# Kernel tuning notes

Hardware: AMD Instinct MI355X
Metric: run time of the kernel (lower is better)

## Reference

```python
import jax, jax.numpy as jnp
import numpy as np
import math

S = 128
EPS = 1e-05

def _rope_seq(x):
    # x: [B, L, 2, s]; rope over dim=1 (sequence), matching torch rope(x, dim=1)
    B, L, two, s = x.shape
    half = s // 2
    pos = jnp.arange(L, dtype=jnp.float32)[:, None]              # [L,1] (one unsqueeze)
    inv_freq = 10000.0 ** (jnp.arange(half, dtype=jnp.float32) / half)
    sinusoid = pos[..., None] * inv_freq[None, None, :]          # [L,1,half]
    sin = jnp.sin(sinusoid)
    cos = jnp.cos(sinusoid)
    x1, x2 = jnp.split(x, 2, axis=-1)
    return jnp.concatenate([x1 * cos - x2 * sin, x2 * cos + x1 * sin], axis=-1)

def setup_inputs() -> dict:
    key = jax.random.key(0)
    ks = jax.random.split(key, 8)
    B, L, D = 8, 1024, 1024
    E = 2 * D
    x = jax.random.normal(ks[0], (B, L, D), dtype=jnp.float32)
    g = jnp.ones((1,), dtype=jnp.float32)
    uv_w = jax.random.normal(ks[1], (2 * E + S, D), dtype=jnp.float32) * 0.02
    gamma = jax.random.uniform(ks[2], (2, S), dtype=jnp.float32)
    beta = jax.random.uniform(ks[3], (2, S), dtype=jnp.float32)
    w_rel = jax.random.uniform(ks[4], (2 * L - 1,), dtype=jnp.float32)
    o_w = jax.random.normal(ks[5], (D, E), dtype=jnp.float32) * 0.02
    res_scale = jnp.ones((D,), dtype=jnp.float32)
    return {"x": x, "g": g, "uv_w": uv_w, "gamma": gamma, "beta": beta,
            "w_rel": w_rel, "o_w": o_w, "res_scale": res_scale}

def reference(x, g, uv_w, gamma, beta, w_rel, o_w, res_scale):
    B, L, D = x.shape
    E = (uv_w.shape[0] - S) // 2
    sqrt_s = math.sqrt(S)
    # ScaleNorm
    norm = jnp.linalg.norm(x, axis=-1, keepdims=True) * (D ** -0.5)
    xn = x / jnp.maximum(norm, EPS) * g
    # gated projection + activation
    uv = jax.nn.silu(xn @ uv_w.T)                               # [B,L,2E+S]
    u = uv[..., :E]
    v = uv[..., E:2 * E]
    base = uv[..., 2 * E:]                                       # [B,L,S]
    base = base[:, :, None, :] * gamma[None, None] + beta        # [B,L,2,S]
    base = _rope_seq(base)
    q = base[:, :, 0]                                            # [B,L,S]
    k = base[:, :, 1]
    qk = jnp.einsum('bis,bjs->bij', q, k)                        # [B,L,L]
    # Toeplitz relative bias: bias[i,j] = w_rel[j - i + L - 1]
    idx = jnp.arange(L)[None, :] - jnp.arange(L)[:, None] + (L - 1)
    qk = qk + w_rel[idx][None]
    kernel = jnp.square(jax.nn.relu(qk / sqrt_s))
    out = u * jnp.einsum('bij,bje->bie', kernel, v)              # [B,L,E]
    out = out @ o_w.T                                            # [B,L,D]
    return x * res_scale + out
```

## Files before the change

### kernel.cpp

```cpp
#include <hip/hip_runtime.h>
#include <hip/hip_bf16.h>
#include <math.h>


typedef __hip_bfloat16 bf16;
using v8s = __attribute__((ext_vector_type(8))) short;
using v4f = __attribute__((ext_vector_type(4))) float;
typedef unsigned short u16;

#define BTCH 8
#define LSEQ 1024
#define DDIM 1024
#define EDIM 2048
#define SDIM 128
#define UVN  4224
#define SLABW 4096
#define BUFW  (4 * SLABW)

__device__ __forceinline__ float ldany(const void* p, size_t i, int bf) {
  return bf ? __bfloat162float(((const bf16*)p)[i]) : ((const float*)p)[i];
}
__device__ __forceinline__ void stany(void* p, size_t i, float v, int bf) {
  if (bf) ((bf16*)p)[i] = __float2bfloat16(v);
  else    ((float*)p)[i] = v;
}
__device__ __forceinline__ u16 f2bf(float x) {
  bf16 b = __float2bfloat16(x);
  return *reinterpret_cast<u16*>(&b);
}
__device__ __forceinline__ float bf2f(u16 u) {
  return __uint_as_float((unsigned)u << 16);
}
__device__ __forceinline__ float silu(float v) {
  return v / (1.0f + __expf(-v));
}

__device__ __forceinline__ void xcd_swz(int& bx, int& by) {
  const int W = gridDim.x;
  const int G = W * gridDim.y;
  const int orig = blockIdx.y * W + blockIdx.x;
  const int xcd = orig & 7;
  const int local = orig >> 3;
  const int chunk = G >> 3;
  if ((G & 7) == 0 && chunk % W == 0) {
    const int R = chunk / W;
    bx = local / R;
    by = xcd * R + local % R;
  } else {
    const int q = G >> 3, r = G & 7;
    const int nid = (xcd < r ? xcd * (q + 1) : r * (q + 1) + (xcd - r) * q)
                    + local;
    bx = nid % W;
    by = nid / W;
  }
}

__device__ __forceinline__ void gld16(const u16* g, u16* l) {
  __builtin_amdgcn_global_load_lds(
      (const __attribute__((address_space(1))) void*)g,
      (__attribute__((address_space(3))) void*)l, 16, 0, 0);
}

__device__ __forceinline__ const v8s* swz_rd(const u16* slab, int row, int q) {
  return (const v8s*)(slab + row * 32 + ((q ^ ((row >> 1) & 3)) << 3));
}

__global__ void detect_kernel(const u16* g16, int* flag) {
  *flag = (g16[0] == 0x3F80) ? 1 : 0;
}

__global__ __launch_bounds__(256) void wsplit_kernel(const void* __restrict__ w,
                                                     u16* __restrict__ whi,
                                                     u16* __restrict__ wlo,
                                                     const int* __restrict__ flagp,
                                                     int n) {
  const int bf = *flagp;
  const size_t i = ((size_t)blockIdx.x * 256 + threadIdx.x) * 8;
  if (i >= (size_t)n) return;
  if (bf) {
    *(uint4*)(whi + i) = *(const uint4*)((const u16*)w + i);
  } else {
    const float* wf = (const float*)w;
    float t[8];
    *(float4*)&t[0] = *(const float4*)(wf + i);
    *(float4*)&t[4] = *(const float4*)(wf + i + 4);
    u16 h[8], l[8];
    #pragma unroll
    for (int j = 0; j < 8; j++) {
      h[j] = f2bf(t[j]);
      l[j] = f2bf(t[j] - bf2f(h[j]));
    }
    *(uint4*)(whi + i) = *(uint4*)&h[0];
    *(uint4*)(wlo + i) = *(uint4*)&l[0];
  }
}

__global__ __launch_bounds__(256) void rmsnorm_kernel(const void* __restrict__ x,
                                                      const void* __restrict__ g,
                                                      u16* __restrict__ xnhi,
                                                      u16* __restrict__ xnlo,
                                                      const int* __restrict__ flagp,
                                                      unsigned long long row0) {
  const int bf = *flagp;
  const int m = blockIdx.x;
  const size_t gbase = (row0 + m) * DDIM;
  float ss = 0.f;
  float vals[4];
  #pragma unroll
  for (int i = 0; i < 4; i++) {
    vals[i] = ldany(x, gbase + threadIdx.x + i * 256, bf);
    ss += vals[i] * vals[i];
  }
  #pragma unroll
  for (int o = 32; o > 0; o >>= 1) ss += __shfl_down(ss, o);
  __shared__ float red[5];
  if ((threadIdx.x & 63) == 0) red[threadIdx.x >> 6] = ss;
  __syncthreads();
  if (threadIdx.x == 0) {
    float tot = red[0] + red[1] + red[2] + red[3];
    float rms = sqrtf(tot * (1.0f / DDIM));
    red[4] = ldany(g, 0, bf) / fmaxf(rms, 1e-5f);
  }
  __syncthreads();
  const float scale = red[4];
  #pragma unroll
  for (int i = 0; i < 4; i++) {
    const size_t idx = (size_t)m * DDIM + threadIdx.x + i * 256;
    float v = vals[i] * scale;
    u16 h = f2bf(v);
    xnhi[idx] = h;
    xnlo[idx] = f2bf(v - bf2f(h));
  }
}

__device__ __forceinline__ void mfma_core(u16* __restrict__ sm,
                                          const u16* __restrict__ AhiG,
                                          const u16* __restrict__ AloG, int lda,
                                          const u16* __restrict__ BhiG,
                                          const u16* __restrict__ BloG, int ldb,
                                          int use_blo, int K, v4f acc[4][4]) {
  const int tid = threadIdx.x;
  const int w = tid >> 6, lane = tid & 63, quad = lane >> 4, lr = lane & 15;
  const int wr = w >> 1, wc = w & 1;
  const int sr0 = w * 16 + (lane >> 2);
  const int sch = lane & 3;

  auto stage = [&](int buf, int kk) {
    u16* lbase = sm + buf * BUFW + w * 512;
    #pragma unroll
    for (int c = 0; c < 2; c++) {
      const int r = sr0 + c * 64;
      const int sc = sch ^ ((r >> 1) & 3);
      u16* ld = lbase + c * 2048;
      const size_t oa = (size_t)r * lda + kk + sc * 8;
      const size_t ob = (size_t)r * ldb + kk + sc * 8;
      gld16(AhiG + oa, ld);
      gld16(AloG + oa, ld + SLABW);
      gld16(BhiG + ob, ld + 2 * SLABW);
      if (use_blo) gld16(BloG + ob, ld + 3 * SLABW);
    }
  };

  stage(0, 0);
  __syncthreads();
  int cur = 0;
  for (int k0 = 0; k0 < K; k0 += 32) {
    if (k0 + 32 < K) stage(cur ^ 1, k0 + 32);
    const u16* sA = sm + cur * BUFW;
    v8s aH[4], aL[4], bh[4], bl[4];
    #pragma unroll
    for (int rt = 0; rt < 4; rt++) {
      const int row = wr * 64 + rt * 16 + lr;
      aH[rt] = *swz_rd(sA, row, quad);
      aL[rt] = *swz_rd(sA + SLABW, row, quad);
    }
    #pragma unroll
    for (int ct = 0; ct < 4; ct++) {
      const int brow = wc * 64 + ct * 16 + lr;
      bh[ct] = *swz_rd(sA + 2 * SLABW, brow, quad);
      if (use_blo) bl[ct] = *swz_rd(sA + 3 * SLABW, brow, quad);
    }
    #pragma unroll
    for (int ct = 0; ct < 4; ct++) {
      #pragma unroll
      for (int rt = 0; rt < 4; rt++)
        acc[rt][ct] = __builtin_amdgcn_mfma_f32_16x16x32_bf16(aH[rt], bh[ct], acc[rt][ct], 0, 0, 0);
      #pragma unroll
      for (int rt = 0; rt < 4; rt++)
        acc[rt][ct] = __builtin_amdgcn_mfma_f32_16x16x32_bf16(aL[rt], bh[ct], acc[rt][ct], 0, 0, 0);
      if (use_blo) {
        #pragma unroll
        for (int rt = 0; rt < 4; rt++)
          acc[rt][ct] = __builtin_amdgcn_mfma_f32_16x16x32_bf16(aH[rt], bl[ct], acc[rt][ct], 0, 0, 0);
      }
    }
    __syncthreads();
    cur ^= 1;
  }
}

template <typename F>
__device__ __forceinline__ void epilogue_rows(const v4f acc[4][4], F body) {
  const int tid = threadIdx.x;
  const int w = tid >> 6, lane = tid & 63;
  const int quad = lane >> 4, lr = lane & 15;
  const int wr = w >> 1, wc = w & 1;
  #pragma unroll
  for (int rt = 0; rt < 4; rt++)
    #pragma unroll
    for (int rg = 0; rg < 4; rg++) {
      const int lrow = wr * 64 + rt * 16 + quad * 4 + rg;
      #pragma unroll
      for (int ct = 0; ct < 4; ct++) {
        const int lcol = wc * 64 + ct * 16 + lr;
        body(lrow, lcol, acc[rt][ct][rg]);
      }
    }
}

__global__ __launch_bounds__(256) void gemm_uv_kernel(const u16* __restrict__ xnhi,
                                                      const u16* __restrict__ xnlo,
                                                      const u16* __restrict__ uvwhi,
                                                      const u16* __restrict__ uvwlo,
                                                      float* __restrict__ u,
                                                      u16* __restrict__ vThi,
                                                      u16* __restrict__ vTlo,
                                                      float* __restrict__ base,
                                                      const int* __restrict__ flagp) {
  __shared__ __align__(16) u16 sm[2 * BUFW];
  const int bf = *flagp;
  int bxi, byi;
  xcd_swz(bxi, byi);
  const int bm = byi * 128, bn = bxi * 128;
  v4f acc[4][4];
  #pragma unroll
  for (int rt = 0; rt < 4; rt++)
    #pragma unroll
    for (int ct = 0; ct < 4; ct++) acc[rt][ct] = (v4f){0.f, 0.f, 0.f, 0.f};
  mfma_core(sm, xnhi + (size_t)bm * DDIM, xnlo + (size_t)bm * DDIM, DDIM,
            uvwhi + (size_t)bn * DDIM, uvwlo + (size_t)bn * DDIM, DDIM,
            bf ? 0 : 1, DDIM, acc);

  if (bn < EDIM) {
    epilogue_rows(acc, [&](int lrow, int lcol, float av) {
      u[(size_t)(bm + lrow) * EDIM + bn + lcol] = silu(av);
    });
  } else if (bn < 2 * EDIM) {
    const int z = bm >> 10, l0 = bm & (LSEQ - 1), e0 = bn - EDIM;
    const int tid = threadIdx.x;
    #pragma unroll
    for (int pass = 0; pass < 2; pass++) {
      __syncthreads();
      epilogue_rows(acc, [&](int lrow, int lcol, float av) {
        const float v = silu(av);
        const u16 hh = f2bf(v);
        sm[lcol * 136 + lrow] = pass ? f2bf(v - bf2f(hh)) : hh;
      });
      __syncthreads();
      u16* dst = pass ? vTlo : vThi;
      const int c = tid >> 1, part = tid & 1;
      const uint4* srcp = (const uint4*)(sm + c * 136 + part * 64);
      uint4* dstp = (uint4*)(dst + ((size_t)z * EDIM + e0 + c) * LSEQ + l0 + part * 64);
      #pragma unroll
      for (int j = 0; j < 8; j++) dstp[j] = srcp[j];
    }
  } else {
    epilogue_rows(acc, [&](int lrow, int lcol, float av) {
      base[(size_t)(bm + lrow) * SDIM + (bn - 2 * EDIM) + lcol] = silu(av);
    });
  }
}

__global__ __launch_bounds__(64) void rope_kernel(const float* __restrict__ base,
                                                  const void* __restrict__ gamma,
                                                  const void* __restrict__ beta,
                                                  u16* __restrict__ qhi,
                                                  u16* __restrict__ qlo,
                                                  u16* __restrict__ khi,
                                                  u16* __restrict__ klo,
                                                  const int* __restrict__ flagp) {
  const int bf = *flagp;
  const int m = blockIdx.x;
  const int pos = m & (LSEQ - 1);
  const int j = threadIdx.x;
  double f = pow(10000.0, (double)j / 64.0);
  double ds, dc;
  sincos((double)pos * f, &ds, &dc);
  const float s = (float)ds, c = (float)dc;
  const float b1 = base[(size_t)m * SDIM + j];
  const float b2 = base[(size_t)m * SDIM + 64 + j];
  {
    float x1 = b1 * ldany(gamma, j, bf) + ldany(beta, j, bf);
    float x2 = b2 * ldany(gamma, 64 + j, bf) + ldany(beta, 64 + j, bf);
    float o1 = x1 * c - x2 * s, o2 = x2 * c + x1 * s;
    u16 h1 = f2bf(o1), h2 = f2bf(o2);
    qhi[(size_t)m * SDIM + j] = h1;      qlo[(size_t)m * SDIM + j] = f2bf(o1 - bf2f(h1));
    qhi[(size_t)m * SDIM + 64 + j] = h2; qlo[(size_t)m * SDIM + 64 + j] = f2bf(o2 - bf2f(h2));
  }
  {
    float x1 = b1 * ldany(gamma, SDIM + j, bf) + ldany(beta, SDIM + j, bf);
    float x2 = b2 * ldany(gamma, SDIM + 64 + j, bf) + ldany(beta, SDIM + 64 + j, bf);
    float o1 = x1 * c - x2 * s, o2 = x2 * c + x1 * s;
    u16 h1 = f2bf(o1), h2 = f2bf(o2);
    khi[(size_t)m * SDIM + j] = h1;      klo[(size_t)m * SDIM + j] = f2bf(o1 - bf2f(h1));
    khi[(size_t)m * SDIM + 64 + j] = h2; klo[(size_t)m * SDIM + 64 + j] = f2bf(o2 - bf2f(h2));
  }
}

__global__ __launch_bounds__(256) void gemm_qk_kernel(const u16* __restrict__ qhi,
                                                      const u16* __restrict__ qlo,
                                                      const u16* __restrict__ khi,
                                                      const u16* __restrict__ klo,
                                                      const void* __restrict__ w_rel,
                                                      u16* __restrict__ kerhi,
                                                      u16* __restrict__ kerlo,
                                                      const int* __restrict__ flagp) {
  __shared__ __align__(16) u16 sm[2 * BUFW];
  const int bf = *flagp;
  const int z = blockIdx.z;
  int bxi, byi;
  xcd_swz(bxi, byi);
  const int bm = byi * 128, bn = bxi * 128;
  v4f acc[4][4];
  #pragma unroll
  for (int rt = 0; rt < 4; rt++)
    #pragma unroll
    for (int ct = 0; ct < 4; ct++) acc[rt][ct] = (v4f){0.f, 0.f, 0.f, 0.f};
  const size_t ao = ((size_t)z * LSEQ + bm) * SDIM;
  const size_t bo = ((size_t)z * LSEQ + bn) * SDIM;
  mfma_core(sm, qhi + ao, qlo + ao, SDIM, khi + bo, klo + bo, SDIM, 1, SDIM, acc);
  const float inv_sqrt_s = 0.08838834764831845f;
  epilogue_rows(acc, [&](int lrow, int lcol, float av) {
    const int gi = bm + lrow, gj = bn + lcol;
    float v = av + ldany(w_rel, gj - gi + (LSEQ - 1), bf);
    v = fmaxf(v, 0.f) * inv_sqrt_s;
    v = v * v;
    const u16 hh = f2bf(v);
    const size_t idx = ((size_t)z * LSEQ + gi) * LSEQ + gj;
    kerhi[idx] = hh;
    kerlo[idx] = f2bf(v - bf2f(hh));
  });
}

__global__ __launch_bounds__(256) void gemm_av_kernel(const u16* __restrict__ kerhi,
                                                      const u16* __restrict__ kerlo,
                                                      const u16* __restrict__ vThi,
                                                      const u16* __restrict__ vTlo,
                                                      const float* __restrict__ u,
                                                      u16* __restrict__ out2hi,
                                                      u16* __restrict__ out2lo) {
  __shared__ __align__(16) u16 sm[2 * BUFW];
  const int z = blockIdx.z;
  int bxi, byi;
  xcd_swz(bxi, byi);
  const int bm = byi * 128, bn = bxi * 128;
  v4f acc[4][4];
  #pragma unroll
  for (int rt = 0; rt < 4; rt++)
    #pragma unroll
    for (int ct = 0; ct < 4; ct++) acc[rt][ct] = (v4f){0.f, 0.f, 0.f, 0.f};
  const size_t ao = ((size_t)z * LSEQ + bm) * LSEQ;
  const size_t bo = ((size_t)z * EDIM + bn) * LSEQ;
  mfma_core(sm, kerhi + ao, kerlo + ao, LSEQ, vThi + bo, vTlo + bo, LSEQ,
            1, LSEQ, acc);
  epilogue_rows(acc, [&](int lrow, int lcol, float av) {
    const size_t grow = (size_t)z * LSEQ + bm + lrow;
    const float v = av * u[grow * EDIM + bn + lcol];
    const u16 hh = f2bf(v);
    out2hi[grow * EDIM + bn + lcol] = hh;
    out2lo[grow * EDIM + bn + lcol] = f2bf(v - bf2f(hh));
  });
}

__global__ __launch_bounds__(256) void gemm_out_kernel(const u16* __restrict__ out2hi,
                                                       const u16* __restrict__ out2lo,
                                                       const u16* __restrict__ owhi,
                                                       const u16* __restrict__ owlo,
                                                       const void* __restrict__ x,
                                                       const void* __restrict__ res_scale,
                                                       void* __restrict__ out,
                                                       const int* __restrict__ flagp,
                                                       unsigned long long row0) {
  __shared__ __align__(16) u16 sm[2 * BUFW];
  const int bf = *flagp;
  int bxi, byi;
  xcd_swz(bxi, byi);
  const int bm = byi * 128, bn = bxi * 128;
  v4f acc[4][4];
  #pragma unroll
  for (int rt = 0; rt < 4; rt++)
    #pragma unroll
    for (int ct = 0; ct < 4; ct++) acc[rt][ct] = (v4f){0.f, 0.f, 0.f, 0.f};
  mfma_core(sm, out2hi + (size_t)bm * EDIM, out2lo + (size_t)bm * EDIM, EDIM,
            owhi + (size_t)bn * EDIM, owlo + (size_t)bn * EDIM, EDIM,
            bf ? 0 : 1, EDIM, acc);
  epilogue_rows(acc, [&](int lrow, int lcol, float av) {
    const size_t gidx = (row0 + bm + lrow) * DDIM + bn + lcol;
    float v = av + ldany(x, gidx, bf) * ldany(res_scale, bn + lcol, bf);
    stany(out, gidx, v, bf);
  });
}

extern "C" void kernel_launch(void* const* d_in, const int* in_sizes, int n_in,
                              void* d_out, int out_size, void* d_ws, size_t ws_size,
                              hipStream_t stream) {
  const void* x         = d_in[0];
  const void* g         = d_in[1];
  const void* uv_w      = d_in[2];
  const void* gamma     = d_in[3];
  const void* beta      = d_in[4];
  const void* w_rel     = d_in[5];
  const void* o_w       = d_in[6];
  const void* res_scale = d_in[7];

  char* ws = (char*)d_ws;
  size_t off = 0;
  int* flag = (int*)(ws + off); off += 256;
  u16* uvwhi = (u16*)(ws + off); off += (size_t)UVN * DDIM * 2;
  u16* uvwlo = (u16*)(ws + off); off += (size_t)UVN * DDIM * 2;
  u16* owhi  = (u16*)(ws + off); off += (size_t)DDIM * EDIM * 2;
  u16* owlo  = (u16*)(ws + off); off += (size_t)DDIM * EDIM * 2;

  int nb = 1;
  for (int cand = 8; cand >= 1; cand >>= 1) {
    size_t need = off + (size_t)cand * 35127296ULL;
    if (ws_size >= need) { nb = cand; break; }
  }
  const int rows = nb * LSEQ;

  u16*   xnhi = (u16*)(ws + off); off += (size_t)rows * DDIM * 2;
  u16*   xnlo = (u16*)(ws + off); off += (size_t)rows * DDIM * 2;
  float* u    = (float*)(ws + off); off += (size_t)rows * EDIM * 4;
  float* base = (float*)(ws + off); off += (size_t)rows * SDIM * 4;
  u16*   qhi  = (u16*)(ws + off); off += (size_t)rows * SDIM * 2;
  u16*   qlo  = (u16*)(ws + off); off += (size_t)rows * SDIM * 2;
  u16*   khi  = (u16*)(ws + off); off += (size_t)rows * SDIM * 2;
  u16*   klo  = (u16*)(ws + off); off += (size_t)rows * SDIM * 2;
  u16*   kerhi= (u16*)(ws + off); off += (size_t)nb * LSEQ * LSEQ * 2;
  u16*   kerlo= (u16*)(ws + off); off += (size_t)nb * LSEQ * LSEQ * 2;
  u16*   vThi = (u16*)(ws + off); off += (size_t)nb * EDIM * LSEQ * 2;
  u16*   vTlo = (u16*)(ws + off); off += (size_t)nb * EDIM * LSEQ * 2;
  u16*   o2hi = (u16*)(ws + off); off += (size_t)rows * EDIM * 2;
  u16*   o2lo = (u16*)(ws + off); off += (size_t)rows * EDIM * 2;

  detect_kernel<<<1, 1, 0, stream>>>((const u16*)g, flag);
  wsplit_kernel<<<(UVN * DDIM) / (8 * 256), 256, 0, stream>>>(uv_w, uvwhi, uvwlo,
                                                              flag, UVN * DDIM);
  wsplit_kernel<<<(DDIM * EDIM) / (8 * 256), 256, 0, stream>>>(o_w, owhi, owlo,
                                                               flag, DDIM * EDIM);

  for (int b = 0; b < BTCH / nb; b++) {
    const unsigned long long row0 = (unsigned long long)b * rows;

    rmsnorm_kernel<<<rows, 256, 0, stream>>>(x, g, xnhi, xnlo, flag, row0);
    {
      dim3 grid(UVN / 128, rows / 128);
      gemm_uv_kernel<<<grid, 256, 0, stream>>>(xnhi, xnlo, uvwhi, uvwlo, u,
                                               vThi, vTlo, base, flag);
    }
    rope_kernel<<<rows, 64, 0, stream>>>(base, gamma, beta, qhi, qlo, khi, klo, flag);
    {
      dim3 grid(LSEQ / 128, LSEQ / 128, nb);
      gemm_qk_kernel<<<grid, 256, 0, stream>>>(qhi, qlo, khi, klo, w_rel,
                                               kerhi, kerlo, flag);
    }
    {
      dim3 grid(EDIM / 128, LSEQ / 128, nb);
      gemm_av_kernel<<<grid, 256, 0, stream>>>(kerhi, kerlo, vThi, vTlo, u,
                                               o2hi, o2lo);
    }
    {
      dim3 grid(DDIM / 128, rows / 128);
      gemm_out_kernel<<<grid, 256, 0, stream>>>(o2hi, o2lo, owhi, owlo, x,
                                                res_scale, d_out, flag, row0);
    }
  }
}
```

Before: 669.0 us.

## Load A operand directly from global into registers, stage only B in LDS

The shared GEMM core now stages only the B operand (hi/lo) through LDS. Each wave reads its A fragments (hi and lo) straight from global memory into registers, double-buffered across two k-steps with a loop unrolled by two. This halves LDS footprint and LDS read traffic and should allow higher occupancy. The cost is more register pressure and uncoalesced-ish 16-byte global loads for A. The A rows are also duplicated across the two column-waves, and the loop assumes K is a multiple of 64.

```diff
diff --git a/kernel.cpp b/kernel.cpp
--- a/kernel.cpp
+++ b/kernel.cpp
@@ -15,7 +15,7 @@
 #define SDIM 128
 #define UVN  4224
 #define SLABW 4096
-#define BUFW  (4 * SLABW)
+#define BUFB  (2 * SLABW)
 
 __device__ __forceinline__ float ldany(const void* p, size_t i, int bf) {
   return bf ? __bfloat162float(((const bf16*)p)[i]) : ((const float*)p)[i];
@@ -145,57 +145,59 @@
   const int sr0 = w * 16 + (lane >> 2);
   const int sch = lane & 3;
 
-  auto stage = [&](int buf, int kk) {
-    u16* lbase = sm + buf * BUFW + w * 512;
+  auto stageB = [&](int buf, int kk) {
+    u16* lbase = sm + buf * BUFB + w * 512;
     #pragma unroll
     for (int c = 0; c < 2; c++) {
       const int r = sr0 + c * 64;
       const int sc = sch ^ ((r >> 1) & 3);
       u16* ld = lbase + c * 2048;
-      const size_t oa = (size_t)r * lda + kk + sc * 8;
       const size_t ob = (size_t)r * ldb + kk + sc * 8;
-      gld16(AhiG + oa, ld);
-      gld16(AloG + oa, ld + SLABW);
-      gld16(BhiG + ob, ld + 2 * SLABW);
-      if (use_blo) gld16(BloG + ob, ld + 3 * SLABW);
+      gld16(BhiG + ob, ld);
+      if (use_blo) gld16(BloG + ob, ld + SLABW);
     }
   };
 
-  stage(0, 0);
-  __syncthreads();
-  int cur = 0;
-  for (int k0 = 0; k0 < K; k0 += 32) {
-    if (k0 + 32 < K) stage(cur ^ 1, k0 + 32);
-    const u16* sA = sm + cur * BUFW;
-    v8s aH[4], aL[4], bh[4], bl[4];
+  auto prefA = [&](v8s aH[4], v8s aL[4], int kk) {
     #pragma unroll
     for (int rt = 0; rt < 4; rt++) {
-      const int row = wr * 64 + rt * 16 + lr;
-      aH[rt] = *swz_rd(sA, row, quad);
-      aL[rt] = *swz_rd(sA + SLABW, row, quad);
-    }
+      const size_t ro = (size_t)(wr * 64 + rt * 16 + lr) * lda + kk + quad * 8;
+      aH[rt] = *(const v8s*)(AhiG + ro);
+      aL[rt] = *(const v8s*)(AloG + ro);
+    }
+  };
+
+  auto compute = [&](const u16* sB, const v8s aH[4], const v8s aL[4]) {
     #pragma unroll
     for (int ct = 0; ct < 4; ct++) {
       const int brow = wc * 64 + ct * 16 + lr;
-      bh[ct] = *swz_rd(sA + 2 * SLABW, brow, quad);
-      if (use_blo) bl[ct] = *swz_rd(sA + 3 * SLABW, brow, quad);
-    }
-    #pragma unroll
-    for (int ct = 0; ct < 4; ct++) {
+      const v8s bh = *swz_rd(sB, brow, quad);
       #pragma unroll
       for (int rt = 0; rt < 4; rt++)
-        acc[rt][ct] = __builtin_amdgcn_mfma_f32_16x16x32_bf16(aH[rt], bh[ct], acc[rt][ct], 0, 0, 0);
+        acc[rt][ct] = __builtin_amdgcn_mfma_f32_16x16x32_bf16(aH[rt], bh, acc[rt][ct], 0, 0, 0);
       #pragma unroll
       for (int rt = 0; rt < 4; rt++)
-        acc[rt][ct] = __builtin_amdgcn_mfma_f32_16x16x32_bf16(aL[rt], bh[ct], acc[rt][ct], 0, 0, 0);
+        acc[rt][ct] = __builtin_amdgcn_mfma_f32_16x16x32_bf16(aL[rt], bh, acc[rt][ct], 0, 0, 0);
       if (use_blo) {
+        const v8s bl = *swz_rd(sB + SLABW, brow, quad);
         #pragma unroll
         for (int rt = 0; rt < 4; rt++)
-          acc[rt][ct] = __builtin_amdgcn_mfma_f32_16x16x32_bf16(aH[rt], bl[ct], acc[rt][ct], 0, 0, 0);
+          acc[rt][ct] = __builtin_amdgcn_mfma_f32_16x16x32_bf16(aH[rt], bl, acc[rt][ct], 0, 0, 0);
       }
     }
+  };
+
+  v8s a0H[4], a0L[4], a1H[4], a1L[4];
+  prefA(a0H, a0L, 0);
+  stageB(0, 0);
+  __syncthreads();
+  for (int k0 = 0; k0 < K; k0 += 64) {
+    if (k0 + 32 < K) { stageB(1, k0 + 32); prefA(a1H, a1L, k0 + 32); }
+    compute(sm, a0H, a0L);
     __syncthreads();
-    cur ^= 1;
+    if (k0 + 64 < K) { stageB(0, k0 + 64); prefA(a0H, a0L, k0 + 64); }
+    compute(sm + BUFB, a1H, a1L);
+    __syncthreads();
   }
 }
 
@@ -227,7 +229,7 @@
                                                       u16* __restrict__ vTlo,
                                                       float* __restrict__ base,
                                                       const int* __restrict__ flagp) {
-  __shared__ __align__(16) u16 sm[2 * BUFW];
+  __shared__ __align__(16) u16 sm[17408];
   const int bf = *flagp;
   int bxi, byi;
   xcd_swz(bxi, byi);
@@ -315,7 +317,7 @@
                                                       u16* __restrict__ kerhi,
                                                       u16* __restrict__ kerlo,
                                                       const int* __restrict__ flagp) {
-  __shared__ __align__(16) u16 sm[2 * BUFW];
+  __shared__ __align__(16) u16 sm[2 * BUFB];
   const int bf = *flagp;
   const int z = blockIdx.z;
   int bxi, byi;
@@ -349,7 +351,7 @@
                                                       const float* __restrict__ u,
                                                       u16* __restrict__ out2hi,
                                                       u16* __restrict__ out2lo) {
-  __shared__ __align__(16) u16 sm[2 * BUFW];
+  __shared__ __align__(16) u16 sm[2 * BUFB];
   const int z = blockIdx.z;
   int bxi, byi;
   xcd_swz(bxi, byi);
@@ -381,7 +383,7 @@
                                                        void* __restrict__ out,
                                                        const int* __restrict__ flagp,
                                                        unsigned long long row0) {
-  __shared__ __align__(16) u16 sm[2 * BUFW];
+  __shared__ __align__(16) u16 sm[2 * BUFB];
   const int bf = *flagp;
   int bxi, byi;
   xcd_swz(bxi, byi);
```

After: 1.054 ms. 57.6% more time.
